# Performance work log

Hardware: AMD Instinct MI355X
Metric: run time of the kernel (lower is better)

## Reference

```python
import jax, jax.numpy as jnp
import numpy as np

EPS = 1e-12

def _sn(w, u):
    # spectral norm, num_svs=1, num_itrs=1, eval mode (power iteration is
    # under no_grad in the original, so sv is a constant w.r.t. autodiff)
    Wm = w.reshape(w.shape[0], -1)          # [out, in*kh*kw]
    v = u @ Wm                               # [1, in*kh*kw]
    v = v / jnp.maximum(jnp.linalg.norm(v), EPS)
    u2 = v @ Wm.T                            # [1, out]
    u2 = u2 / jnp.maximum(jnp.linalg.norm(u2), EPS)
    sv = jnp.squeeze(v @ Wm.T @ u2.T)        # top singular value estimate
    return w / jax.lax.stop_gradient(sv)


def setup_inputs() -> dict:
    key = jax.random.key(0)
    ks = jax.random.split(key, 10)
    B, C, H, W = 32, 512, 64, 64
    Cr = C // 8
    return {
        'x':  jax.random.normal(ks[0], (B, C, H, W), jnp.float32),
        'w1': jax.random.normal(ks[1], (Cr, C, 1, 1), jnp.float32) * 0.05,
        'b1': jax.random.normal(ks[2], (Cr,), jnp.float32) * 0.02,
        'u1': jax.random.normal(ks[3], (1, Cr), jnp.float32),
        'w2': jax.random.normal(ks[4], (C, Cr, 1, 1), jnp.float32) * 0.05,
        'b2': jax.random.normal(ks[5], (C,), jnp.float32) * 0.02,
        'u2': jax.random.normal(ks[6], (1, C), jnp.float32),
        'w3': jax.random.normal(ks[7], (1, 2, 3, 3), jnp.float32) * 0.1,
        'b3': jax.random.normal(ks[8], (1,), jnp.float32) * 0.02,
        'u3': jax.random.normal(ks[9], (1, 1), jnp.float32),
    }


def reference(x, w1, b1, u1, w2, b2, u2, w3, b3, u3):
    # --- channel attention ---
    W1 = _sn(w1, u1).reshape(w1.shape[0], w1.shape[1])   # [Cr, C]
    W2 = _sn(w2, u2).reshape(w2.shape[0], w2.shape[1])   # [C, Cr]
    avg = jnp.mean(x, axis=(2, 3))                        # [B, C]
    mx  = jnp.max(x, axis=(2, 3))                         # [B, C]
    a = jax.nn.relu(avg @ W1.T + b1) @ W2.T + b2          # [B, C]
    m = jax.nn.relu(mx  @ W1.T + b1) @ W2.T + b2          # [B, C]
    s = jax.nn.sigmoid(a + m)
    x = x * s[:, :, None, None]
    # --- spatial attention ---
    ca = jnp.mean(x, axis=1, keepdims=True)               # [B,1,H,W]
    cm = jnp.max(x, axis=1, keepdims=True)                # [B,1,H,W]
    cat = jnp.concatenate([ca, cm], axis=1)               # [B,2,H,W]
    W3 = _sn(w3, u3)
    y = jax.lax.conv_general_dilated(
        cat, W3, window_strides=(1, 1), padding=((1, 1), (1, 1)),
        dimension_numbers=('NCHW', 'OIHW', 'NCHW'))
    y = y + b3.reshape(1, -1, 1, 1)
    return x * jax.nn.sigmoid(y)
```

## Files before the change

kernel.cpp:

```cpp
#include <hip/hip_runtime.h>


#define B_   32
#define C_   512
#define CR_  64
#define HW_  4096
#define WID_ 64
#define EPSF 1e-12f

__device__ __forceinline__ float sigmoidf(float x) {
  return 1.0f / (1.0f + __expf(-x));
}

__global__ __launch_bounds__(256) void pool_kernel(const float* __restrict__ x,
                                                   float* __restrict__ avg,
                                                   float* __restrict__ mx) {
  const int plane = blockIdx.x;
  const int t = threadIdx.x;
  const float4* xp = (const float4*)(x + (size_t)plane * HW_);
  float s = 0.0f, m = -INFINITY;
  #pragma unroll
  for (int q = 0; q < 4; q++) {
    float4 a = xp[q * 256 + t];
    s += (a.x + a.y) + (a.z + a.w);
    m = fmaxf(m, fmaxf(fmaxf(a.x, a.y), fmaxf(a.z, a.w)));
  }
  for (int o = 32; o > 0; o >>= 1) {
    s += __shfl_down(s, o);
    m = fmaxf(m, __shfl_down(m, o));
  }
  __shared__ float rs[4], rm[4];
  int wave = t >> 6, lane = t & 63;
  if (lane == 0) { rs[wave] = s; rm[wave] = m; }
  __syncthreads();
  if (t == 0) {
    float S = rs[0] + rs[1] + rs[2] + rs[3];
    float M = fmaxf(fmaxf(rm[0], rm[1]), fmaxf(rm[2], rm[3]));
    avg[plane] = S * (1.0f / HW_);
    mx[plane] = M;
  }
}

__device__ __forceinline__ float block_reduce_sum(float v, float* red) {
  int t = threadIdx.x;
  red[t] = v;
  __syncthreads();
  for (int o = 128; o > 0; o >>= 1) {
    if (t < o) red[t] += red[t + o];
    __syncthreads();
  }
  float r = red[0];
  __syncthreads();
  return r;
}

__global__ __launch_bounds__(256) void sv_kernel(const float* __restrict__ w1, const float* __restrict__ u1,
                                                 const float* __restrict__ w2, const float* __restrict__ u2,
                                                 const float* __restrict__ w3, const float* __restrict__ u3,
                                                 float* __restrict__ sv) {
  __shared__ float v[C_];
  __shared__ float red[256];
  __shared__ float tmp[C_];
  const int t = threadIdx.x;
  const int blk = blockIdx.x;

  if (blk == 0) {
    if (t < CR_) tmp[t] = u1[t];
    __syncthreads();
    float ax = 0.0f, ay = 0.0f;
    for (int i = 0; i < CR_; i++) {
      float ui = tmp[i];
      float2 wv = *(const float2*)(w1 + (size_t)i * C_ + 2 * t);
      ax += ui * wv.x; ay += ui * wv.y;
    }
    v[2 * t] = ax; v[2 * t + 1] = ay;
    float nv = block_reduce_sum(ax * ax + ay * ay, red);
    float dv = fmaxf(sqrtf(nv), EPSF);
    int i = t >> 2, part = t & 3;
    const float4* wr = (const float4*)(w1 + (size_t)i * C_ + part * 128);
    float acc = 0.0f;
    #pragma unroll 8
    for (int q = 0; q < 32; q++) {
      float4 wv = wr[q];
      int j = part * 128 + 4 * q;
      acc += v[j] * wv.x + v[j + 1] * wv.y + v[j + 2] * wv.z + v[j + 3] * wv.w;
    }
    acc += __shfl_down(acc, 2);
    acc += __shfl_down(acc, 1);
    float q2 = 0.0f;
    if (part == 0) { float a2 = acc / dv; q2 = a2 * a2; }
    float nt2 = block_reduce_sum(q2, red);
    if (t == 0) sv[0] = nt2 / fmaxf(sqrtf(nt2), EPSF);

  } else if (blk == 1) {
    for (int i = t; i < C_; i += 256) tmp[i] = u2[i];
    __syncthreads();
    int j = t & 63, ig = t >> 6;
    const float* wp = w2 + (size_t)ig * 128 * CR_ + j;
    float a = 0.0f;
    #pragma unroll 8
    for (int i = 0; i < 128; i++) a += tmp[ig * 128 + i] * wp[(size_t)i * CR_];
    red[t] = a;
    __syncthreads();
    if (t < CR_) v[t] = red[t] + red[t + 64] + red[t + 128] + red[t + 192];
    __syncthreads();
    float p = (t < CR_) ? v[t] * v[t] : 0.0f;
    float nv = block_reduce_sum(p, red);
    float dv = fmaxf(sqrtf(nv), EPSF);
    float q = 0.0f;
    #pragma unroll
    for (int rep = 0; rep < 2; rep++) {
      int i = t + rep * 256;
      const float4* wr = (const float4*)(w2 + (size_t)i * CR_);
      float acc = 0.0f;
      #pragma unroll
      for (int qq = 0; qq < 16; qq++) {
        float4 wv = wr[qq];
        acc += v[4 * qq] * wv.x + v[4 * qq + 1] * wv.y +
               v[4 * qq + 2] * wv.z + v[4 * qq + 3] * wv.w;
      }
      acc /= dv;
      q += acc * acc;
    }
    float nt2 = block_reduce_sum(q, red);
    if (t == 0) sv[1] = nt2 / fmaxf(sqrtf(nt2), EPSF);

  } else {
    if (t == 0) {
      float u3v = u3[0];
      float nvs = 0.0f;
      for (int k = 0; k < 18; k++) { float vv = u3v * w3[k]; nvs += vv * vv; }
      float d = fmaxf(sqrtf(nvs), EPSF);
      float tt = 0.0f;
      for (int k = 0; k < 18; k++) tt += (u3v * w3[k] / d) * w3[k];
      float u2n = tt / fmaxf(fabsf(tt), EPSF);
      sv[2] = tt * u2n;
    }
  }
}

__global__ __launch_bounds__(256) void mlp_kernel(const float* __restrict__ avg, const float* __restrict__ mx,
                                                  const float* __restrict__ w1, const float* __restrict__ b1,
                                                  const float* __restrict__ w2, const float* __restrict__ b2,
                                                  const float* __restrict__ sv, float* __restrict__ s) {
  const int b = blockIdx.x;
  const int t = threadIdx.x;
  __shared__ float pool[2][C_];
  __shared__ float hid[2][CR_];
  for (int i = t; i < C_; i += 256) {
    pool[0][i] = avg[b * C_ + i];
    pool[1][i] = mx[b * C_ + i];
  }
  __syncthreads();
  const float inv1 = 1.0f / sv[0];
  const float inv2 = 1.0f / sv[1];
  if (t < 2 * CR_) {
    int kind = t >> 6;
    int i = t & 63;
    const float4* wr = (const float4*)(w1 + (size_t)i * C_);
    float acc = 0.0f;
    for (int qq = 0; qq < C_ / 4; qq++) {
      float4 u = wr[qq];
      acc += pool[kind][qq * 4 + 0] * u.x + pool[kind][qq * 4 + 1] * u.y +
             pool[kind][qq * 4 + 2] * u.z + pool[kind][qq * 4 + 3] * u.w;
    }
    hid[kind][i] = fmaxf(acc * inv1 + b1[i], 0.0f);
  }
  __syncthreads();
  for (int c = t; c < C_; c += 256) {
    const float* wr = w2 + (size_t)c * CR_;
    float aa = 0.0f, mm = 0.0f;
    #pragma unroll 8
    for (int i = 0; i < CR_; i++) {
      float wv = wr[i];
      aa += hid[0][i] * wv;
      mm += hid[1][i] * wv;
    }
    float val = (aa + mm) * inv2 + 2.0f * b2[c];
    s[b * C_ + c] = sigmoidf(val);
  }
}

__global__ __launch_bounds__(1024) void scale_pool_kernel(const float* __restrict__ x,
                                                          const float* __restrict__ s,
                                                          float* __restrict__ ca,
                                                          float* __restrict__ cm) {
  const int b = blockIdx.y;
  const int hw0 = blockIdx.x * 512;
  const int t = threadIdx.x;
  const int pxid = t & 255;
  const int cg = t >> 8;
  __shared__ float srow[C_];
  for (int i = t; i < C_; i += 1024) srow[i] = s[b * C_ + i];
  __syncthreads();
  const int px = hw0 + pxid * 2;
  const float* xb = x + (size_t)b * C_ * HW_ + px;
  float s0 = 0.f, s1 = 0.f, m0 = -INFINITY, m1 = -INFINITY;
  const int c0 = cg * 128;
  #pragma unroll 8
  for (int c = c0; c < c0 + 128; c++) {
    float2 u = *(const float2*)(xb + (size_t)c * HW_);
    float sc = srow[c];
    float v0 = u.x * sc, v1 = u.y * sc;
    s0 += v0; s1 += v1;
    m0 = fmaxf(m0, v0); m1 = fmaxf(m1, v1);
  }
  __shared__ float rs0[4][256], rs1[4][256], rm0[4][256], rm1[4][256];
  rs0[cg][pxid] = s0; rs1[cg][pxid] = s1;
  rm0[cg][pxid] = m0; rm1[cg][pxid] = m1;
  __syncthreads();
  if (cg == 0) {
    float S0 = rs0[0][pxid] + rs0[1][pxid] + rs0[2][pxid] + rs0[3][pxid];
    float S1 = rs1[0][pxid] + rs1[1][pxid] + rs1[2][pxid] + rs1[3][pxid];
    float M0 = fmaxf(fmaxf(rm0[0][pxid], rm0[1][pxid]), fmaxf(rm0[2][pxid], rm0[3][pxid]));
    float M1 = fmaxf(fmaxf(rm1[0][pxid], rm1[1][pxid]), fmaxf(rm1[2][pxid], rm1[3][pxid]));
    *(float2*)(ca + (size_t)b * HW_ + px) = make_float2(S0 * (1.0f / C_), S1 * (1.0f / C_));
    *(float2*)(cm + (size_t)b * HW_ + px) = make_float2(M0, M1);
  }
}

__global__ __launch_bounds__(256) void conv_sy_kernel(const float* __restrict__ ca,
                                                      const float* __restrict__ cm,
                                                      const float* __restrict__ w3,
                                                      const float* __restrict__ b3,
                                                      const float* __restrict__ sv,
                                                      float* __restrict__ sy) {
  const int b = blockIdx.y;
  const int hw0 = blockIdx.x * 512;
  const int t = threadIdx.x;
  const float inv3 = 1.0f / sv[2];
  float wn[18];
  #pragma unroll
  for (int k = 0; k < 18; k++) wn[k] = w3[k] * inv3;
  const float b3f = b3[0];

  #pragma unroll
  for (int e = 0; e < 2; e++) {
    int px = hw0 + t * 2 + e;
    int h = px >> 6, w = px & 63;
    float acc = b3f;
    #pragma unroll
    for (int dh = -1; dh <= 1; dh++) {
      int hh = h + dh;
      if (hh < 0 || hh >= 64) continue;
      #pragma unroll
      for (int dw = -1; dw <= 1; dw++) {
        int ww = w + dw;
        if (ww < 0 || ww >= WID_) continue;
        int n = b * HW_ + hh * WID_ + ww;
        int k = (dh + 1) * 3 + (dw + 1);
        acc += ca[n] * wn[k] + cm[n] * wn[9 + k];
      }
    }
    sy[b * HW_ + px] = sigmoidf(acc);
  }
}

__global__ __launch_bounds__(256) void out_kernel(const float* __restrict__ x,
                                                  const float* __restrict__ s,
                                                  const float* __restrict__ sy,
                                                  float* __restrict__ out) {
  const size_t N4 = (size_t)B_ * C_ * HW_ / 4;
  const size_t stride = (size_t)gridDim.x * blockDim.x;
  for (size_t i = (size_t)blockIdx.x * blockDim.x + threadIdx.x; i < N4; i += stride) {
    size_t base = i * 4;
    int hw = (int)(base & (HW_ - 1));
    int bc = (int)(base >> 12);
    int b  = bc >> 9;
    float sc = s[bc];
    float4 u = ((const float4*)x)[i];
    float4 g = *(const float4*)(sy + (size_t)b * HW_ + hw);
    float4 r;
    r.x = u.x * sc * g.x;
    r.y = u.y * sc * g.y;
    r.z = u.z * sc * g.z;
    r.w = u.w * sc * g.w;
    ((float4*)out)[i] = r;
  }
}

extern "C" void kernel_launch(void* const* d_in, const int* in_sizes, int n_in,
                              void* d_out, int out_size, void* d_ws, size_t ws_size,
                              hipStream_t stream) {
  const float* x  = (const float*)d_in[0];
  const float* w1 = (const float*)d_in[1];
  const float* b1 = (const float*)d_in[2];
  const float* u1 = (const float*)d_in[3];
  const float* w2 = (const float*)d_in[4];
  const float* b2 = (const float*)d_in[5];
  const float* u2 = (const float*)d_in[6];
  const float* w3 = (const float*)d_in[7];
  const float* b3 = (const float*)d_in[8];
  const float* u3 = (const float*)d_in[9];

  float* ws = (float*)d_ws;
  float* avg = ws;
  float* mx  = ws + 16384;
  float* s   = ws + 32768;
  float* sv  = ws + 49152;
  float* ca  = ws + 65536;
  float* cm  = ws + 196608;
  float* sy  = ws + 327680;

  pool_kernel<<<B_ * C_, 256, 0, stream>>>(x, avg, mx);
  sv_kernel<<<3, 256, 0, stream>>>(w1, u1, w2, u2, w3, u3, sv);
  mlp_kernel<<<B_, 256, 0, stream>>>(avg, mx, w1, b1, w2, b2, sv, s);
  scale_pool_kernel<<<dim3(8, B_), 1024, 0, stream>>>(x, s, ca, cm);
  conv_sy_kernel<<<dim3(8, B_), 256, 0, stream>>>(ca, cm, w3, b3, sv, sy);
  out_kernel<<<2048, 256, 0, stream>>>(x, s, sy, (float*)d_out);
}
```

Before: 584.1 us.

## Fuse spectral-norm estimation into MLP and conv kernels, retile pooling kernels

The standalone sv_kernel is removed. The power-iteration estimates for W1 and W2 are now recomputed redundantly inside each mlp block, which is split across 4 channel quarters per batch. The W3 estimate is computed inside conv_sy_kernel. pool_kernel now gives each wave its own plane, removing the shared-memory and barrier reduction, and scale_pool_kernel uses 256-thread blocks with float4 loads over 128-pixel tiles, giving more blocks in flight. This cuts one launch and raises parallelism in the channel-MLP and pooling stages, at the cost of redundant weight reads and matvecs in every MLP block.

Result: no change. 583.7 us (-0.1%).

```diff
diff --git a/kernel.cpp b/kernel.cpp
--- a/kernel.cpp
+++ b/kernel.cpp
@@ -15,29 +15,24 @@
 __global__ __launch_bounds__(256) void pool_kernel(const float* __restrict__ x,
                                                    float* __restrict__ avg,
                                                    float* __restrict__ mx) {
-  const int plane = blockIdx.x;
-  const int t = threadIdx.x;
+  const int plane = blockIdx.x * 4 + (threadIdx.x >> 6);
+  const int lane = threadIdx.x & 63;
   const float4* xp = (const float4*)(x + (size_t)plane * HW_);
   float s = 0.0f, m = -INFINITY;
   #pragma unroll
-  for (int q = 0; q < 4; q++) {
-    float4 a = xp[q * 256 + t];
+  for (int q = 0; q < 16; q++) {
+    float4 a = xp[q * 64 + lane];
     s += (a.x + a.y) + (a.z + a.w);
     m = fmaxf(m, fmaxf(fmaxf(a.x, a.y), fmaxf(a.z, a.w)));
   }
+  #pragma unroll
   for (int o = 32; o > 0; o >>= 1) {
     s += __shfl_down(s, o);
     m = fmaxf(m, __shfl_down(m, o));
   }
-  __shared__ float rs[4], rm[4];
-  int wave = t >> 6, lane = t & 63;
-  if (lane == 0) { rs[wave] = s; rm[wave] = m; }
-  __syncthreads();
-  if (t == 0) {
-    float S = rs[0] + rs[1] + rs[2] + rs[3];
-    float M = fmaxf(fmaxf(rm[0], rm[1]), fmaxf(rm[2], rm[3]));
-    avg[plane] = S * (1.0f / HW_);
-    mx[plane] = M;
+  if (lane == 0) {
+    avg[plane] = s * (1.0f / HW_);
+    mx[plane] = m;
   }
 }
 
@@ -54,28 +49,33 @@
   return r;
 }
 
-__global__ __launch_bounds__(256) void sv_kernel(const float* __restrict__ w1, const float* __restrict__ u1,
-                                                 const float* __restrict__ w2, const float* __restrict__ u2,
-                                                 const float* __restrict__ w3, const float* __restrict__ u3,
-                                                 float* __restrict__ sv) {
+__global__ __launch_bounds__(256) void mlp_kernel(const float* __restrict__ avg, const float* __restrict__ mx,
+                                                  const float* __restrict__ w1, const float* __restrict__ b1,
+                                                  const float* __restrict__ u1,
+                                                  const float* __restrict__ w2, const float* __restrict__ b2,
+                                                  const float* __restrict__ u2,
+                                                  float* __restrict__ s) {
+  const int b = blockIdx.y;
+  const int qtr = blockIdx.x;
+  const int t = threadIdx.x;
   __shared__ float v[C_];
   __shared__ float red[256];
-  __shared__ float tmp[C_];
-  const int t = threadIdx.x;
-  const int blk = blockIdx.x;
-
-  if (blk == 0) {
-    if (t < CR_) tmp[t] = u1[t];
-    __syncthreads();
-    float ax = 0.0f, ay = 0.0f;
-    for (int i = 0; i < CR_; i++) {
-      float ui = tmp[i];
-      float2 wv = *(const float2*)(w1 + (size_t)i * C_ + 2 * t);
-      ax += ui * wv.x; ay += ui * wv.y;
-    }
-    v[2 * t] = ax; v[2 * t + 1] = ay;
-    float nv = block_reduce_sum(ax * ax + ay * ay, red);
-    float dv = fmaxf(sqrtf(nv), EPSF);
+  __shared__ float pool2[2][C_];
+  __shared__ float hid[2][CR_];
+
+  if (t < CR_) hid[0][t] = u1[t];
+  __syncthreads();
+  float ax = 0.0f, ay = 0.0f;
+  #pragma unroll 8
+  for (int i = 0; i < CR_; i++) {
+    float ui = hid[0][i];
+    float2 wv = *(const float2*)(w1 + (size_t)i * C_ + 2 * t);
+    ax += ui * wv.x; ay += ui * wv.y;
+  }
+  v[2 * t] = ax; v[2 * t + 1] = ay;
+  float nv = block_reduce_sum(ax * ax + ay * ay, red);
+  float dv = fmaxf(sqrtf(nv), EPSF);
+  {
     int i = t >> 2, part = t & 3;
     const float4* wr = (const float4*)(w1 + (size_t)i * C_ + part * 128);
     float acc = 0.0f;
@@ -89,24 +89,27 @@
     acc += __shfl_down(acc, 1);
     float q2 = 0.0f;
     if (part == 0) { float a2 = acc / dv; q2 = a2 * a2; }
-    float nt2 = block_reduce_sum(q2, red);
-    if (t == 0) sv[0] = nt2 / fmaxf(sqrtf(nt2), EPSF);
-
-  } else if (blk == 1) {
-    for (int i = t; i < C_; i += 256) tmp[i] = u2[i];
-    __syncthreads();
+    nv = block_reduce_sum(q2, red);
+  }
+  const float inv1 = fmaxf(sqrtf(nv), EPSF) / nv;
+
+  for (int i = t; i < C_; i += 256) pool2[0][i] = u2[i];
+  __syncthreads();
+  {
     int j = t & 63, ig = t >> 6;
     const float* wp = w2 + (size_t)ig * 128 * CR_ + j;
     float a = 0.0f;
     #pragma unroll 8
-    for (int i = 0; i < 128; i++) a += tmp[ig * 128 + i] * wp[(size_t)i * CR_];
+    for (int i = 0; i < 128; i++) a += pool2[0][ig * 128 + i] * wp[(size_t)i * CR_];
     red[t] = a;
-    __syncthreads();
-    if (t < CR_) v[t] = red[t] + red[t + 64] + red[t + 128] + red[t + 192];
-    __syncthreads();
-    float p = (t < CR_) ? v[t] * v[t] : 0.0f;
-    float nv = block_reduce_sum(p, red);
-    float dv = fmaxf(sqrtf(nv), EPSF);
+  }
+  __syncthreads();
+  if (t < CR_) v[t] = red[t] + red[t + 64] + red[t + 128] + red[t + 192];
+  __syncthreads();
+  float p = (t < CR_) ? v[t] * v[t] : 0.0f;
+  nv = block_reduce_sum(p, red);
+  dv = fmaxf(sqrtf(nv), EPSF);
+  {
     float q = 0.0f;
     #pragma unroll
     for (int rep = 0; rep < 2; rep++) {
@@ -122,100 +125,87 @@
       acc /= dv;
       q += acc * acc;
     }
-    float nt2 = block_reduce_sum(q, red);
-    if (t == 0) sv[1] = nt2 / fmaxf(sqrtf(nt2), EPSF);
-
-  } else {
-    if (t == 0) {
-      float u3v = u3[0];
-      float nvs = 0.0f;
-      for (int k = 0; k < 18; k++) { float vv = u3v * w3[k]; nvs += vv * vv; }
-      float d = fmaxf(sqrtf(nvs), EPSF);
-      float tt = 0.0f;
-      for (int k = 0; k < 18; k++) tt += (u3v * w3[k] / d) * w3[k];
-      float u2n = tt / fmaxf(fabsf(tt), EPSF);
-      sv[2] = tt * u2n;
-    }
-  }
-}
-
-__global__ __launch_bounds__(256) void mlp_kernel(const float* __restrict__ avg, const float* __restrict__ mx,
-                                                  const float* __restrict__ w1, const float* __restrict__ b1,
-                                                  const float* __restrict__ w2, const float* __restrict__ b2,
-                                                  const float* __restrict__ sv, float* __restrict__ s) {
-  const int b = blockIdx.x;
-  const int t = threadIdx.x;
-  __shared__ float pool[2][C_];
-  __shared__ float hid[2][CR_];
+    nv = block_reduce_sum(q, red);
+  }
+  const float inv2 = fmaxf(sqrtf(nv), EPSF) / nv;
+
   for (int i = t; i < C_; i += 256) {
-    pool[0][i] = avg[b * C_ + i];
-    pool[1][i] = mx[b * C_ + i];
-  }
-  __syncthreads();
-  const float inv1 = 1.0f / sv[0];
-  const float inv2 = 1.0f / sv[1];
+    pool2[0][i] = avg[b * C_ + i];
+    pool2[1][i] = mx[b * C_ + i];
+  }
+  __syncthreads();
   if (t < 2 * CR_) {
     int kind = t >> 6;
     int i = t & 63;
     const float4* wr = (const float4*)(w1 + (size_t)i * C_);
     float acc = 0.0f;
+    #pragma unroll 8
     for (int qq = 0; qq < C_ / 4; qq++) {
       float4 u = wr[qq];
-      acc += pool[kind][qq * 4 + 0] * u.x + pool[kind][qq * 4 + 1] * u.y +
-             pool[kind][qq * 4 + 2] * u.z + pool[kind][qq * 4 + 3] * u.w;
+      acc += pool2[kind][qq * 4 + 0] * u.x + pool2[kind][qq * 4 + 1] * u.y +
+             pool2[kind][qq * 4 + 2] * u.z + pool2[kind][qq * 4 + 3] * u.w;
     }
     hid[kind][i] = fmaxf(acc * inv1 + b1[i], 0.0f);
   }
   __syncthreads();
-  for (int c = t; c < C_; c += 256) {
-    const float* wr = w2 + (size_t)c * CR_;
+  if (t < 128) {
+    int c = qtr * 128 + t;
+    const float4* wr = (const float4*)(w2 + (size_t)c * CR_);
     float aa = 0.0f, mm = 0.0f;
-    #pragma unroll 8
-    for (int i = 0; i < CR_; i++) {
-      float wv = wr[i];
-      aa += hid[0][i] * wv;
-      mm += hid[1][i] * wv;
+    #pragma unroll
+    for (int k = 0; k < 16; k++) {
+      float4 wv = wr[k];
+      aa += hid[0][4 * k] * wv.x + hid[0][4 * k + 1] * wv.y +
+            hid[0][4 * k + 2] * wv.z + hid[0][4 * k + 3] * wv.w;
+      mm += hid[1][4 * k] * wv.x + hid[1][4 * k + 1] * wv.y +
+            hid[1][4 * k + 2] * wv.z + hid[1][4 * k + 3] * wv.w;
     }
     float val = (aa + mm) * inv2 + 2.0f * b2[c];
     s[b * C_ + c] = sigmoidf(val);
   }
 }
 
-__global__ __launch_bounds__(1024) void scale_pool_kernel(const float* __restrict__ x,
-                                                          const float* __restrict__ s,
-                                                          float* __restrict__ ca,
-                                                          float* __restrict__ cm) {
+__global__ __launch_bounds__(256) void scale_pool_kernel(const float* __restrict__ x,
+                                                         const float* __restrict__ s,
+                                                         float* __restrict__ ca,
+                                                         float* __restrict__ cm) {
   const int b = blockIdx.y;
-  const int hw0 = blockIdx.x * 512;
+  const int hw0 = blockIdx.x * 128;
   const int t = threadIdx.x;
-  const int pxid = t & 255;
-  const int cg = t >> 8;
+  const int pxs = t & 31;
+  const int cg = t >> 5;
   __shared__ float srow[C_];
-  for (int i = t; i < C_; i += 1024) srow[i] = s[b * C_ + i];
-  __syncthreads();
-  const int px = hw0 + pxid * 2;
+  for (int i = t; i < C_; i += 256) srow[i] = s[b * C_ + i];
+  __syncthreads();
+  const int px = hw0 + pxs * 4;
   const float* xb = x + (size_t)b * C_ * HW_ + px;
-  float s0 = 0.f, s1 = 0.f, m0 = -INFINITY, m1 = -INFINITY;
-  const int c0 = cg * 128;
+  float4 sm = make_float4(0.f, 0.f, 0.f, 0.f);
+  float4 mxv = make_float4(-INFINITY, -INFINITY, -INFINITY, -INFINITY);
+  const int c0 = cg * 64;
   #pragma unroll 8
-  for (int c = c0; c < c0 + 128; c++) {
-    float2 u = *(const float2*)(xb + (size_t)c * HW_);
+  for (int c = c0; c < c0 + 64; c++) {
+    float4 u = *(const float4*)(xb + (size_t)c * HW_);
     float sc = srow[c];
-    float v0 = u.x * sc, v1 = u.y * sc;
-    s0 += v0; s1 += v1;
-    m0 = fmaxf(m0, v0); m1 = fmaxf(m1, v1);
-  }
-  __shared__ float rs0[4][256], rs1[4][256], rm0[4][256], rm1[4][256];
-  rs0[cg][pxid] = s0; rs1[cg][pxid] = s1;
-  rm0[cg][pxid] = m0; rm1[cg][pxid] = m1;
-  __syncthreads();
-  if (cg == 0) {
-    float S0 = rs0[0][pxid] + rs0[1][pxid] + rs0[2][pxid] + rs0[3][pxid];
-    float S1 = rs1[0][pxid] + rs1[1][pxid] + rs1[2][pxid] + rs1[3][pxid];
-    float M0 = fmaxf(fmaxf(rm0[0][pxid], rm0[1][pxid]), fmaxf(rm0[2][pxid], rm0[3][pxid]));
-    float M1 = fmaxf(fmaxf(rm1[0][pxid], rm1[1][pxid]), fmaxf(rm1[2][pxid], rm1[3][pxid]));
-    *(float2*)(ca + (size_t)b * HW_ + px) = make_float2(S0 * (1.0f / C_), S1 * (1.0f / C_));
-    *(float2*)(cm + (size_t)b * HW_ + px) = make_float2(M0, M1);
+    float v0 = u.x * sc, v1 = u.y * sc, v2 = u.z * sc, v3 = u.w * sc;
+    sm.x += v0; sm.y += v1; sm.z += v2; sm.w += v3;
+    mxv.x = fmaxf(mxv.x, v0); mxv.y = fmaxf(mxv.y, v1);
+    mxv.z = fmaxf(mxv.z, v2); mxv.w = fmaxf(mxv.w, v3);
+  }
+  __shared__ float4 rs[8][32], rm[8][32];
+  rs[cg][pxs] = sm; rm[cg][pxs] = mxv;
+  __syncthreads();
+  if (t < 32) {
+    float4 S = rs[0][t], M = rm[0][t];
+    #pragma unroll
+    for (int g = 1; g < 8; g++) {
+      float4 a = rs[g][t], m2 = rm[g][t];
+      S.x += a.x; S.y += a.y; S.z += a.z; S.w += a.w;
+      M.x = fmaxf(M.x, m2.x); M.y = fmaxf(M.y, m2.y);
+      M.z = fmaxf(M.z, m2.z); M.w = fmaxf(M.w, m2.w);
+    }
+    S.x *= (1.0f / C_); S.y *= (1.0f / C_); S.z *= (1.0f / C_); S.w *= (1.0f / C_);
+    *(float4*)(ca + (size_t)b * HW_ + hw0 + t * 4) = S;
+    *(float4*)(cm + (size_t)b * HW_ + hw0 + t * 4) = M;
   }
 }
 
@@ -223,12 +213,24 @@
                                                       const float* __restrict__ cm,
                                                       const float* __restrict__ w3,
                                                       const float* __restrict__ b3,
-                                                      const float* __restrict__ sv,
+                                                      const float* __restrict__ u3,
                                                       float* __restrict__ sy) {
   const int b = blockIdx.y;
   const int hw0 = blockIdx.x * 512;
   const int t = threadIdx.x;
-  const float inv3 = 1.0f / sv[2];
+  __shared__ float ssv3;
+  if (t == 0) {
+    float u3v = u3[0];
+    float nvs = 0.0f;
+    for (int k = 0; k < 18; k++) { float vv = u3v * w3[k]; nvs += vv * vv; }
+    float d = fmaxf(sqrtf(nvs), EPSF);
+    float tt = 0.0f;
+    for (int k = 0; k < 18; k++) tt += (u3v * w3[k] / d) * w3[k];
+    float u2n = tt / fmaxf(fabsf(tt), EPSF);
+    ssv3 = tt * u2n;
+  }
+  __syncthreads();
+  const float inv3 = 1.0f / ssv3;
   float wn[18];
   #pragma unroll
   for (int k = 0; k < 18; k++) wn[k] = w3[k] * inv3;
@@ -297,15 +299,13 @@
   float* avg = ws;
   float* mx  = ws + 16384;
   float* s   = ws + 32768;
-  float* sv  = ws + 49152;
-  float* ca  = ws + 65536;
-  float* cm  = ws + 196608;
-  float* sy  = ws + 327680;
-
-  pool_kernel<<<B_ * C_, 256, 0, stream>>>(x, avg, mx);
-  sv_kernel<<<3, 256, 0, stream>>>(w1, u1, w2, u2, w3, u3, sv);
-  mlp_kernel<<<B_, 256, 0, stream>>>(avg, mx, w1, b1, w2, b2, sv, s);
-  scale_pool_kernel<<<dim3(8, B_), 1024, 0, stream>>>(x, s, ca, cm);
-  conv_sy_kernel<<<dim3(8, B_), 256, 0, stream>>>(ca, cm, w3, b3, sv, sy);
+  float* ca  = ws + 49152;
+  float* cm  = ws + 180224;
+  float* sy  = ws + 311296;
+
+  pool_kernel<<<B_ * C_ / 4, 256, 0, stream>>>(x, avg, mx);
+  mlp_kernel<<<dim3(4, B_), 256, 0, stream>>>(avg, mx, w1, b1, u1, w2, b2, u2, s);
+  scale_pool_kernel<<<dim3(32, B_), 256, 0, stream>>>(x, s, ca, cm);
+  conv_sy_kernel<<<dim3(8, B_), 256, 0, stream>>>(ca, cm, w3, b3, u3, sy);
   out_kernel<<<2048, 256, 0, stream>>>(x, s, sy, (float*)d_out);
 }
```
